# Kernel tuning notes

Hardware: AMD Instinct MI355X
Metric: run time of the kernel (lower is better)

The kernel has to match this reference:

```python
import jax, jax.numpy as jnp
import numpy as np

B, S, D = 1, 2048, 768
NH = 24; QNOPE = 32; QROPE = 16; QHD = QNOPE + QROPE; VHD = 32
QLR = 384; KVLR = 128
PK_HEADS = 4; KDIM = 128; NEXP = 16384; KNN = 8; EDIM = 768
ACT_HID = 24   # SwiGLU(dim=8): int(2*(4*8)/3)=21 -> rounded up to multiple_of=4 -> 24
SHARED_HID = 3072  # expert_dim * n_shared_experts = 768*4
EPS = 1e-5


def rms_norm(x, w):
    return x * jax.lax.rsqrt(jnp.mean(x * x, -1, keepdims=True) + EPS) * w


def swiglu(x, w1, w2, w3):
    return (jax.nn.silu(x @ w1.T) * (x @ w3.T)) @ w2.T


def rope(t, cos, sin):
    # t: (b, s, h, d); cos/sin: (s, d//2); rotate consecutive pairs (matches apply_rope)
    b, s, h, d = t.shape
    tr = t.reshape(b, s, h, d // 2, 2)
    r, i = tr[..., 0], tr[..., 1]
    c = cos[None, :, None, :]
    sn = sin[None, :, None, :]
    return jnp.stack([r * c - i * sn, r * sn + i * c], -1).reshape(b, s, h, d)


def setup_inputs() -> dict:
    key = jax.random.key(0)
    ks = jax.random.split(key, 20)
    rn = lambda k, shp, sc=0.02: jax.random.normal(k, shp, jnp.float32) * sc
    # RoPE tables: cos/sin of pos * inv_freq, dim = qk_rope_head_dim // 2 = 8
    inv = 1.0 / (10000.0 ** (jnp.arange(0, QROPE, 2, dtype=jnp.float32) / QROPE))
    f = jnp.arange(S, dtype=jnp.float32)[:, None] * inv[None, :]
    # causal additive mask (built here; spec fill 'zeros' is a placeholder)
    mask = jnp.where(jnp.tril(jnp.ones((S, S), bool)), 0.0, -1e9).astype(jnp.float32)[None, None]
    kb = float(1.0 / np.sqrt(KDIM))
    return {
        'x': rn(ks[0], (B, S, D), 1.0),
        'norm1_w': jnp.ones((D,), jnp.float32),
        'q_a_w': rn(ks[1], (QLR, D)),
        'q_a_ln_w': jnp.ones((QLR,), jnp.float32),
        'q_b_w': rn(ks[2], (NH * QHD, QLR)),
        'kv_a_w': rn(ks[3], (KVLR + QROPE, D)),
        'kv_a_ln_w': jnp.ones((KVLR,), jnp.float32),
        'kv_b_w': rn(ks[4], (NH * (QNOPE + VHD), KVLR)),
        'o_w': rn(ks[5], (D, NH * VHD)),
        'norm2_w': jnp.ones((D,), jnp.float32),
        'qp_w': rn(ks[6], (PK_HEADS * KDIM, D)),
        'qp_b': jnp.zeros((PK_HEADS * KDIM,), jnp.float32),
        'bn_g': jnp.ones((PK_HEADS * KDIM,), jnp.float32),
        'bn_b': jnp.zeros((PK_HEADS * KDIM,), jnp.float32),
        'keys': jax.random.uniform(ks[7], (PK_HEADS, NEXP, KDIM), jnp.float32, -kb, kb),
        'aw1': rn(ks[8], (ACT_HID, KNN), 0.1),
        'aw2': rn(ks[9], (KNN, ACT_HID), 0.1),
        'aw3': rn(ks[10], (ACT_HID, KNN), 0.1),
        'w_down': rn(ks[11], (NEXP, EDIM)),
        'w_up': rn(ks[12], (NEXP, EDIM)),
        'sw1': rn(ks[13], (SHARED_HID, D)),
        'sw2': rn(ks[14], (D, SHARED_HID)),
        'sw3': rn(ks[15], (SHARED_HID, D)),
        'mask': mask,
        'freqs_cos': jnp.cos(f),
        'freqs_sin': jnp.sin(f),
    }


def reference(x, norm1_w, q_a_w, q_a_ln_w, q_b_w, kv_a_w, kv_a_ln_w, kv_b_w, o_w,
              norm2_w, qp_w, qp_b, bn_g, bn_b, keys, aw1, aw2, aw3, w_down, w_up,
              sw1, sw2, sw3, mask, freqs_cos, freqs_sin):
    b, s, d = x.shape
    # ---- Attention (MLA-style, pre-norm) ----
    h_in = rms_norm(x, norm1_w)
    q = rms_norm(h_in @ q_a_w.T, q_a_ln_w) @ q_b_w.T
    q = q.reshape(b, s, NH, QHD).transpose(0, 2, 1, 3)            # (b, nh, s, 48)
    q_nope, q_pe = q[..., :QNOPE], q[..., QNOPE:]
    ckv = h_in @ kv_a_w.T                                         # (b, s, 144)
    compressed, k_pe = ckv[..., :KVLR], ckv[..., KVLR:]
    kv = (rms_norm(compressed, kv_a_ln_w) @ kv_b_w.T)
    kv = kv.reshape(b, s, NH, QNOPE + VHD).transpose(0, 2, 1, 3)  # (b, nh, s, 64)
    k_nope, v = kv[..., :QNOPE], kv[..., QNOPE:]
    q_pe = rope(q_pe.transpose(0, 2, 1, 3), freqs_cos, freqs_sin).transpose(0, 2, 1, 3)
    k_pe = rope(k_pe[:, :, None, :], freqs_cos, freqs_sin).transpose(0, 2, 1, 3)  # (b,1,s,16)
    q_states = jnp.concatenate([q_nope, q_pe], -1)                # (b, nh, s, 48)
    k_states = jnp.concatenate([k_nope, jnp.broadcast_to(k_pe, (b, NH, s, QROPE))], -1)
    att = jnp.einsum('bhqd,bhkd->bhqk', q_states, k_states) / np.sqrt(QHD).astype(np.float32) + mask
    probs = jax.nn.softmax(att, -1)
    ctx = jnp.einsum('bhqk,bhkd->bhqd', probs, v).transpose(0, 2, 1, 3).reshape(b, s, NH * VHD)
    h = x + ctx @ o_w.T
    # ---- ALL_MOE (product-key memory FFN) ----
    y = rms_norm(h, norm2_w)
    qflat = y.reshape(-1, d) @ qp_w.T + qp_b
    qflat = qflat / np.sqrt(1.0 + EPS).astype(np.float32) * bn_g + bn_b  # BatchNorm1d eval (mu=0, var=1)
    query = qflat.reshape(b * s, PK_HEADS, KDIM)
    sc = jnp.einsum('nhd,hkd->nhk', query, keys)                  # (b*s, heads, n_keys)
    top_s, top_i = jax.lax.top_k(sc, KNN)                         # (b*s, heads, knn)
    w = jax.nn.softmax(top_s, -1).reshape(b, s, PK_HEADS, KNN)
    idx = top_i.reshape(b, s, PK_HEADS, KNN)
    wd = w_down[idx]                                              # (b, s, heads, knn, D)
    wu = w_up[idx]
    z = jnp.einsum('btd,bthkd->bthk', y, wd)
    z = swiglu(z, aw1, aw2, aw3) * w
    moe = jnp.einsum('bthk,bthkd->btd', z, wu) + swiglu(y, sw1, sw2, sw3)
    return h + moe
```

## Files before the change

### kernel.cpp

```cpp
#include <hip/hip_runtime.h>
#include <hip/hip_bf16.h>
#include <hip/hip_fp16.h>

typedef __hip_bfloat16 bf16;

static constexpr int kS    = 2048;
static constexpr int kD    = 768;
static constexpr int kNH   = 24;
static constexpr int kQHD  = 48;
static constexpr int kVHD  = 32;
static constexpr int kQLR  = 384;
static constexpr int kKVLR = 128;
static constexpr int kPKH  = 4;
static constexpr int kNEXP = 16384;
static constexpr int kSH   = 3072;
static constexpr int kCH   = 768;
static constexpr float kEPS = 1e-5f;

__device__ __forceinline__ float b2f(bf16 v) { return __bfloat162float(v); }
__device__ __forceinline__ float silu_f(float x) { return x / (1.0f + expf(-x)); }

__device__ __forceinline__ float ldf(const void* p, size_t i, int m) {
  if (m == 0) return ((const float*)p)[i];
  if (m == 1) return b2f(((const bf16*)p)[i]);
  return __half2float(((const __half*)p)[i]);
}

__global__ void detect_kernel(const unsigned int* __restrict__ w, int* __restrict__ flag) {
  if (threadIdx.x == 0) {
    unsigned int v = w[0];
    flag[0] = (v == 0x3F800000u) ? 0 : ((v == 0x3C003C00u) ? 2 : 1);
  }
}

__global__ __launch_bounds__(256) void fill_kernel(float* __restrict__ out, float v, int n) {
  int i = blockIdx.x * 256 + threadIdx.x;
  if (i < n) out[i] = v;
}

__global__ __launch_bounds__(256) void rms_in_kernel(
    const void* __restrict__ in, const void* __restrict__ w,
    float* __restrict__ out, int cols, const int* __restrict__ dflag) {
  int m = dflag[0];
  int row = blockIdx.x;
  size_t base = (size_t)row * cols;
  __shared__ float red[256];
  float s = 0.f;
  for (int c = threadIdx.x; c < cols; c += 256) { float v = ldf(in, base + c, m); s += v * v; }
  red[threadIdx.x] = s; __syncthreads();
  for (int o = 128; o > 0; o >>= 1) {
    if (threadIdx.x < o) red[threadIdx.x] += red[threadIdx.x + o];
    __syncthreads();
  }
  float scale = rsqrtf(red[0] / cols + kEPS);
  for (int c = threadIdx.x; c < cols; c += 256)
    out[base + c] = ldf(in, base + c, m) * scale * ldf(w, c, m);
}

__global__ __launch_bounds__(256) void rms_f32_kernel(
    const float* __restrict__ in, int istride, const void* __restrict__ w,
    float* __restrict__ out, int cols, const int* __restrict__ dflag) {
  int m = dflag[0];
  int row = blockIdx.x;
  const float* r = in + (size_t)row * istride;
  __shared__ float red[256];
  float s = 0.f;
  for (int c = threadIdx.x; c < cols; c += 256) { float v = r[c]; s += v * v; }
  red[threadIdx.x] = s; __syncthreads();
  for (int o = 128; o > 0; o >>= 1) {
    if (threadIdx.x < o) red[threadIdx.x] += red[threadIdx.x + o];
    __syncthreads();
  }
  float scale = rsqrtf(red[0] / cols + kEPS);
  for (int c = threadIdx.x; c < cols; c += 256)
    out[(size_t)row * cols + c] = r[c] * scale * ldf(w, c, m);
}

template <bool ACC, int DT>
__device__ __forceinline__ void gemm_body(
    const float* __restrict__ A, int lda,
    const void* __restrict__ W, int ldw, int wrow0, int kofs,
    float* __restrict__ C, int ldc, int N, int K,
    float (*As)[68], float (*Ws)[68]) {
  int row0 = blockIdx.y * 64, col0 = blockIdx.x * 64;
  int tid = threadIdx.x;
  int tx = tid & 15, ty = tid >> 4;
  int am = tid >> 3, ak = (tid & 7) * 4;
  int hn = tid >> 2, hk = (tid & 3) * 8;

  float4 ra0, ra1, rw0, rw1;
  uint4 rh;

  auto fetch = [&](int k0) {
    ra0 = *(const float4*)(A + (size_t)(row0 + am) * lda + k0 + ak);
    ra1 = *(const float4*)(A + (size_t)(row0 + am + 32) * lda + k0 + ak);
    if constexpr (DT == 0) {
      const float* Wf = (const float*)W;
      int n0 = col0 + am, n1 = n0 + 32;
      float4 z = make_float4(0.f, 0.f, 0.f, 0.f);
      rw0 = (n0 < N) ? *(const float4*)(Wf + (size_t)(wrow0 + n0) * ldw + kofs + k0 + ak) : z;
      rw1 = (n1 < N) ? *(const float4*)(Wf + (size_t)(wrow0 + n1) * ldw + kofs + k0 + ak) : z;
    } else {
      int n = col0 + hn;
      if (n < N)
        rh = *(const uint4*)((const unsigned short*)W + (size_t)(wrow0 + n) * ldw + kofs + k0 + hk);
      else
        rh = make_uint4(0u, 0u, 0u, 0u);
    }
  };

  auto stage = [&]() {
    As[ak + 0][am] = ra0.x; As[ak + 1][am] = ra0.y;
    As[ak + 2][am] = ra0.z; As[ak + 3][am] = ra0.w;
    As[ak + 0][am + 32] = ra1.x; As[ak + 1][am + 32] = ra1.y;
    As[ak + 2][am + 32] = ra1.z; As[ak + 3][am + 32] = ra1.w;
    if constexpr (DT == 0) {
      Ws[ak + 0][am] = rw0.x; Ws[ak + 1][am] = rw0.y;
      Ws[ak + 2][am] = rw0.z; Ws[ak + 3][am] = rw0.w;
      Ws[ak + 0][am + 32] = rw1.x; Ws[ak + 1][am + 32] = rw1.y;
      Ws[ak + 2][am + 32] = rw1.z; Ws[ak + 3][am + 32] = rw1.w;
    } else if constexpr (DT == 1) {
      unsigned u[4] = {rh.x, rh.y, rh.z, rh.w};
#pragma unroll
      for (int i = 0; i < 4; i++) {
        Ws[hk + 2 * i][hn]     = __uint_as_float(u[i] << 16);
        Ws[hk + 2 * i + 1][hn] = __uint_as_float(u[i] & 0xFFFF0000u);
      }
    } else {
      unsigned u[4] = {rh.x, rh.y, rh.z, rh.w};
#pragma unroll
      for (int i = 0; i < 4; i++) {
        __half2 h2 = *(__half2*)&u[i];
        float2 f = __half22float2(h2);
        Ws[hk + 2 * i][hn]     = f.x;
        Ws[hk + 2 * i + 1][hn] = f.y;
      }
    }
  };

  float acc[4][4] = {};
  auto compute = [&]() {
#pragma unroll
    for (int kk = 0; kk < 32; kk++) {
      float4 a4 = *(const float4*)&As[kk][ty * 4];
      float4 b4 = *(const float4*)&Ws[kk][tx * 4];
      float a[4] = {a4.x, a4.y, a4.z, a4.w};
      float b[4] = {b4.x, b4.y, b4.z, b4.w};
#pragma unroll
      for (int i = 0; i < 4; i++)
#pragma unroll
        for (int j = 0; j < 4; j++) acc[i][j] += a[i] * b[j];
    }
  };

  fetch(0);
  stage();
  __syncthreads();
  for (int k0 = 32; k0 < K; k0 += 32) {
    fetch(k0);
    compute();
    __syncthreads();
    stage();
    __syncthreads();
  }
  compute();

#pragma unroll
  for (int i = 0; i < 4; i++)
#pragma unroll
    for (int j = 0; j < 4; j++) {
      int col = col0 + tx * 4 + j;
      if (col < N) {
        size_t idx = (size_t)(row0 + ty * 4 + i) * ldc + col;
        C[idx] = (ACC ? C[idx] : 0.f) + acc[i][j];
      }
    }
}

template <bool ACC>
__global__ __launch_bounds__(256) void gemm_kernel(
    const float* __restrict__ A, int lda,
    const void* __restrict__ W, int ldw, int wrow0, int kofs,
    float* __restrict__ C, int ldc,
    int M, int N, int K, const int* __restrict__ dflag) {
  __shared__ float As[32][68];
  __shared__ float Ws[32][68];
  int dm = dflag[0];
  if (dm == 1)      gemm_body<ACC, 1>(A, lda, W, ldw, wrow0, kofs, C, ldc, N, K, As, Ws);
  else if (dm == 0) gemm_body<ACC, 0>(A, lda, W, ldw, wrow0, kofs, C, ldc, N, K, As, Ws);
  else              gemm_body<ACC, 2>(A, lda, W, ldw, wrow0, kofs, C, ldc, N, K, As, Ws);
}

__global__ __launch_bounds__(192) void ropeq_kernel(
    float* __restrict__ q, const void* __restrict__ fc, const void* __restrict__ fs,
    const int* __restrict__ dflag) {
  int m = dflag[0];
  int s = blockIdx.x, t = threadIdx.x;
  int h = t >> 3, p = t & 7;
  float c = ldf(fc, s * 8 + p, m), sn = ldf(fs, s * 8 + p, m);
  size_t base = (size_t)s * (kNH * kQHD) + h * kQHD + 32 + 2 * p;
  float r = q[base], im = q[base + 1];
  q[base]     = r * c - im * sn;
  q[base + 1] = r * sn + im * c;
}

__global__ __launch_bounds__(256) void ropek_kernel(
    const float* __restrict__ ckv, const void* __restrict__ fc, const void* __restrict__ fs,
    float* __restrict__ kpe, const int* __restrict__ dflag) {
  int m = dflag[0];
  int i = blockIdx.x * 256 + threadIdx.x;
  if (i >= kS * 8) return;
  int s = i >> 3, p = i & 7;
  float c = ldf(fc, s * 8 + p, m), sn = ldf(fs, s * 8 + p, m);
  float r  = ckv[(size_t)s * 144 + 128 + 2 * p];
  float im = ckv[(size_t)s * 144 + 128 + 2 * p + 1];
  kpe[s * 16 + 2 * p]     = r * c - im * sn;
  kpe[s * 16 + 2 * p + 1] = r * sn + im * c;
}

__global__ __launch_bounds__(256) void attn_kernel(
    const float* __restrict__ q, const float* __restrict__ kv,
    const float* __restrict__ kpe, float* __restrict__ ctx) {
  constexpr int KT = 64;
  __shared__ float Ks[KT][52];
  __shared__ float Vs[KT][36];
  __shared__ float Pt[KT][33];
  __shared__ float Tm[8][32];
  __shared__ float Sm[8][32];
  __shared__ float Ms[32], Ls[32], Fs[32];
  int qt = blockIdx.x, h = blockIdx.y, t = threadIdx.x;
  int qi = t & 31, g = t >> 5;
  int qrow = qt * 32 + qi;

  float qreg[48];
  const float* qp = q + (size_t)qrow * (kNH * kQHD) + h * kQHD;
#pragma unroll
  for (int i = 0; i < 12; i++) {
    float4 v4 = *(const float4*)(qp + 4 * i);
    qreg[4 * i] = v4.x; qreg[4 * i + 1] = v4.y;
    qreg[4 * i + 2] = v4.z; qreg[4 * i + 3] = v4.w;
  }
  if (t < 32) { Ms[t] = -INFINITY; Ls[t] = 0.f; }
  float acc[4] = {0.f, 0.f, 0.f, 0.f};
  const float scale = 0.144337567297406f;
  int nt = (qt * 32 + 32 + KT - 1) / KT;

  int srow = t >> 2, spart = t & 3;
  for (int tile = 0; tile < nt; tile++) {
    int kbase = tile * KT;
    {
      const float* src = kv + (size_t)(kbase + srow) * (kNH * 64) + h * 64 + spart * 16;
      float4 a = ((const float4*)src)[0];
      float4 b = ((const float4*)src)[1];
      float4 c = ((const float4*)src)[2];
      float4 d = ((const float4*)src)[3];
      if (spart < 2) {
        float* dst = &Ks[srow][spart * 16];
        ((float4*)dst)[0] = a; ((float4*)dst)[1] = b;
        ((float4*)dst)[2] = c; ((float4*)dst)[3] = d;
      } else {
        float* dst = &Vs[srow][(spart - 2) * 16];
        ((float4*)dst)[0] = a; ((float4*)dst)[1] = b;
        ((float4*)dst)[2] = c; ((float4*)dst)[3] = d;
      }
      float4 pe = *(const float4*)(kpe + (size_t)(kbase + srow) * 16 + spart * 4);
      *(float4*)&Ks[srow][32 + spart * 4] = pe;
    }
    __syncthreads();

    float s[8]; float lmax = -INFINITY;
    int k0 = g * 8;
#pragma unroll
    for (int kk = 0; kk < 8; kk++) {
      float d = 0.f;
#pragma unroll
      for (int d4 = 0; d4 < 12; d4++) {
        float4 k4 = *(const float4*)&Ks[k0 + kk][4 * d4];
        d += k4.x * qreg[4 * d4];
        d += k4.y * qreg[4 * d4 + 1];
        d += k4.z * qreg[4 * d4 + 2];
        d += k4.w * qreg[4 * d4 + 3];
      }
      d *= scale;
      if (kbase + k0 + kk > qrow) d = -1e9f;
      s[kk] = d;
      lmax = fmaxf(lmax, d);
    }
    Tm[g][qi] = lmax;
    __syncthreads();

    if (t < 32) {
      float tm = Tm[0][t];
#pragma unroll
      for (int gg = 1; gg < 8; gg++) tm = fmaxf(tm, Tm[gg][t]);
      float mo = Ms[t];
      float mn = fmaxf(mo, tm);
      Fs[t] = expf(mo - mn);
      Ms[t] = mn;
    }
    __syncthreads();

    float mq = Ms[qi];
    float psum = 0.f;
#pragma unroll
    for (int kk = 0; kk < 8; kk++) {
      float e = expf(s[kk] - mq);
      Pt[k0 + kk][qi] = e;
      psum += e;
    }
    Sm[g][qi] = psum;
    __syncthreads();

    if (t < 32) {
      float ls = 0.f;
#pragma unroll
      for (int gg = 0; gg < 8; gg++) ls += Sm[gg][t];
      Ls[t] = Ls[t] * Fs[t] + ls;
    }

    float f = Fs[qi];
#pragma unroll
    for (int j = 0; j < 4; j++) acc[j] *= f;
    int vd0 = g * 4;
#pragma unroll 8
    for (int kk = 0; kk < KT; kk++) {
      float p = Pt[kk][qi];
      float4 v4 = *(const float4*)&Vs[kk][vd0];
      acc[0] += p * v4.x; acc[1] += p * v4.y;
      acc[2] += p * v4.z; acc[3] += p * v4.w;
    }
    __syncthreads();
  }
  float inv = 1.f / Ls[qi];
  float* op = ctx + (size_t)qrow * (kNH * kVHD) + h * kVHD + g * 4;
  op[0] = acc[0] * inv; op[1] = acc[1] * inv;
  op[2] = acc[2] * inv; op[3] = acc[3] * inv;
}

__global__ __launch_bounds__(256) void addx_kernel(
    const void* __restrict__ x, const float* __restrict__ o, float* __restrict__ h, int n,
    const int* __restrict__ dflag) {
  int m = dflag[0];
  int i = blockIdx.x * 256 + threadIdx.x;
  if (i < n) h[i] = ldf(x, i, m) + o[i];
}

__global__ __launch_bounds__(256) void bnq_kernel(
    const float* __restrict__ raw, const void* __restrict__ qp_b,
    const void* __restrict__ g, const void* __restrict__ b,
    float* __restrict__ out, int n, const int* __restrict__ dflag) {
  int m = dflag[0];
  int i = blockIdx.x * 256 + threadIdx.x;
  if (i >= n) return;
  int j = i & 511;
  const float invs = 0.9999950000374996f;
  out[i] = (raw[i] + ldf(qp_b, j, m)) * invs * ldf(g, j, m) + ldf(b, j, m);
}

__global__ __launch_bounds__(256) void convert_keys_kernel(
    const void* __restrict__ keys, float* __restrict__ kf, const int* __restrict__ dflag) {
  int m = dflag[0];
  size_t i = ((size_t)blockIdx.x * 256 + threadIdx.x) * 8;
  if (m == 0) {
    const float4* s = (const float4*)((const float*)keys + i);
    float4 a = s[0], b = s[1];
    *(float4*)(kf + i) = a;
    *(float4*)(kf + i + 4) = b;
  } else if (m == 1) {
    uint4 u = *(const uint4*)((const unsigned short*)keys + i);
    unsigned uu[4] = {u.x, u.y, u.z, u.w};
    float o[8];
#pragma unroll
    for (int j = 0; j < 4; j++) {
      o[2 * j]     = __uint_as_float(uu[j] << 16);
      o[2 * j + 1] = __uint_as_float(uu[j] & 0xFFFF0000u);
    }
    *(float4*)(kf + i)     = make_float4(o[0], o[1], o[2], o[3]);
    *(float4*)(kf + i + 4) = make_float4(o[4], o[5], o[6], o[7]);
  } else {
    uint4 u = *(const uint4*)((const unsigned short*)keys + i);
    unsigned uu[4] = {u.x, u.y, u.z, u.w};
    float o[8];
#pragma unroll
    for (int j = 0; j < 4; j++) {
      __half2 h2 = *(__half2*)&uu[j];
      float2 f = __half22float2(h2);
      o[2 * j] = f.x; o[2 * j + 1] = f.y;
    }
    *(float4*)(kf + i)     = make_float4(o[0], o[1], o[2], o[3]);
    *(float4*)(kf + i + 4) = make_float4(o[4], o[5], o[6], o[7]);
  }
}

__device__ __forceinline__ void pk_tail(
    float* tval, int* tidx, int w, int lane, int n, int h, int rblk,
    float* __restrict__ cv, int* __restrict__ ci,
    float (*ldsv)[64][9], int (*ldsi)[64][9]) {
#pragma unroll
  for (int k = 0; k < 8; k++) { ldsv[w][lane][k] = tval[k]; ldsi[w][lane][k] = tidx[k]; }
  __syncthreads();
  if (w == 0) {
#pragma unroll
    for (int ww = 1; ww < 4; ww++) {
#pragma unroll
      for (int k = 0; k < 8; k++) {
        float cs = ldsv[ww][lane][k]; int cidx = ldsi[ww][lane][k];
        if (cs > tval[7]) {
#pragma unroll
          for (int t = 0; t < 8; t++) {
            if (cs > tval[t]) {
              float tv = tval[t]; int ti = tidx[t];
              tval[t] = cs; tidx[t] = cidx;
              cs = tv; cidx = ti;
            }
          }
        }
      }
    }
    size_t base = ((size_t)(n * 4 + h) * 16 + rblk) * 8;
#pragma unroll
    for (int k = 0; k < 8; k++) { cv[base + k] = tval[k]; ci[base + k] = tidx[k]; }
  }
}

__global__ __launch_bounds__(256) void pk_score_f32_kernel(
    const float* __restrict__ query, const float* __restrict__ keysf,
    float* __restrict__ cv, int* __restrict__ ci) {
  __shared__ float ldsv[4][64][9];
  __shared__ int   ldsi[4][64][9];
  int b    = blockIdx.x;
  int w    = threadIdx.x >> 6, lane = threadIdx.x & 63;
  int rblk = b & 15;
  int h    = (b >> 4) & 3;
  int qb   = b >> 6;
  int n    = qb * 64 + lane;
  int r    = rblk * 4 + w;

  float qv[128];
  const float4* qp = (const float4*)(query + (size_t)n * 512 + h * 128);
#pragma unroll
  for (int i = 0; i < 32; i++) {
    float4 t = qp[i];
    qv[4 * i] = t.x; qv[4 * i + 1] = t.y; qv[4 * i + 2] = t.z; qv[4 * i + 3] = t.w;
  }

  float tval[8]; int tidx[8];
#pragma unroll
  for (int k = 0; k < 8; k++) { tval[k] = -INFINITY; tidx[k] = 0x7FFFFFFF; }

  const float4* hbase = (const float4*)(keysf + (size_t)h * kNEXP * 128);
  int e0 = r * 256;
  for (int e = 0; e < 256; e++) {
    int eu = __builtin_amdgcn_readfirstlane(e0 + e);
    const float4* row = hbase + (size_t)eu * 32;
    float acc = 0.f;
#pragma unroll
    for (int w4 = 0; w4 < 32; w4++) {
      float4 f4 = row[w4];
      acc += f4.x * qv[4 * w4];
      acc += f4.y * qv[4 * w4 + 1];
      acc += f4.z * qv[4 * w4 + 2];
      acc += f4.w * qv[4 * w4 + 3];
    }
    if (acc > tval[7]) {
      float cs = acc; int cidx = eu;
#pragma unroll
      for (int k = 0; k < 8; k++) {
        if (cs > tval[k]) {
          float tv = tval[k]; int ti = tidx[k];
          tval[k] = cs; tidx[k] = cidx;
          cs = tv; cidx = ti;
        }
      }
    }
  }
  pk_tail(tval, tidx, w, lane, n, h, rblk, cv, ci, ldsv, ldsi);
}

template<int M>
__device__ __forceinline__ void pk_score_body(
    const float* __restrict__ query, const void* __restrict__ keys,
    float* __restrict__ cv, int* __restrict__ ci,
    float (*ldsv)[64][9], int (*ldsi)[64][9]) {
  int b    = blockIdx.x;
  int w    = threadIdx.x >> 6, lane = threadIdx.x & 63;
  int rblk = b & 15;
  int h    = (b >> 4) & 3;
  int qb   = b >> 6;
  int n    = qb * 64 + lane;
  int r    = rblk * 4 + w;

  float qv[128];
  const float4* qp = (const float4*)(query + (size_t)n * 512 + h * 128);
#pragma unroll
  for (int i = 0; i < 32; i++) {
    float4 t = qp[i];
    qv[4 * i] = t.x; qv[4 * i + 1] = t.y; qv[4 * i + 2] = t.z; qv[4 * i + 3] = t.w;
  }

  float tval[8]; int tidx[8];
#pragma unroll
  for (int k = 0; k < 8; k++) { tval[k] = -INFINITY; tidx[k] = 0x7FFFFFFF; }

  int e0 = r * 256;
  for (int e = 0; e < 256; e++) {
    int eu = __builtin_amdgcn_readfirstlane(e0 + e);
    float acc = 0.f;
    if constexpr (M == 1) {
      const uint4* row = (const uint4*)((const unsigned*)keys + ((size_t)h * kNEXP + eu) * 64);
#pragma unroll
      for (int w4 = 0; w4 < 16; w4++) {
        uint4 u4 = row[w4];
        unsigned uu[4] = {u4.x, u4.y, u4.z, u4.w};
#pragma unroll
        for (int j = 0; j < 4; j++) {
          float flo = __uint_as_float(uu[j] << 16);
          float fhi = __uint_as_float(uu[j] & 0xFFFF0000u);
          acc += flo * qv[8 * w4 + 2 * j];
          acc += fhi * qv[8 * w4 + 2 * j + 1];
        }
      }
    } else if constexpr (M == 0) {
      const float4* row = (const float4*)((const float*)keys + ((size_t)h * kNEXP + eu) * 128);
#pragma unroll
      for (int w4 = 0; w4 < 32; w4++) {
        float4 f4 = row[w4];
        acc += f4.x * qv[4 * w4];
        acc += f4.y * qv[4 * w4 + 1];
        acc += f4.z * qv[4 * w4 + 2];
        acc += f4.w * qv[4 * w4 + 3];
      }
    } else {
      const uint4* row = (const uint4*)((const unsigned*)keys + ((size_t)h * kNEXP + eu) * 64);
#pragma unroll
      for (int w4 = 0; w4 < 16; w4++) {
        uint4 u4 = row[w4];
        unsigned uu[4] = {u4.x, u4.y, u4.z, u4.w};
#pragma unroll
        for (int j = 0; j < 4; j++) {
          float flo = __half2float(__ushort_as_half((unsigned short)(uu[j] & 0xFFFFu)));
          float fhi = __half2float(__ushort_as_half((unsigned short)(uu[j] >> 16)));
          acc += flo * qv[8 * w4 + 2 * j];
          acc += fhi * qv[8 * w4 + 2 * j + 1];
        }
      }
    }
    if (acc > tval[7]) {
      float cs = acc; int cidx = eu;
#pragma unroll
      for (int k = 0; k < 8; k++) {
        if (cs > tval[k]) {
          float tv = tval[k]; int ti = tidx[k];
          tval[k] = cs; tidx[k] = cidx;
          cs = tv; cidx = ti;
        }
      }
    }
  }
  pk_tail(tval, tidx, w, lane, n, h, rblk, cv, ci, ldsv, ldsi);
}

__global__ __launch_bounds__(256) void pk_score_kernel(
    const float* __restrict__ query, const void* __restrict__ keys,
    float* __restrict__ cv, int* __restrict__ ci, const int* __restrict__ dflag) {
  __shared__ float ldsv[4][64][9];
  __shared__ int   ldsi[4][64][9];
  int m = dflag[0];
  if (m == 1)      pk_score_body<1>(query, keys, cv, ci, ldsv, ldsi);
  else if (m == 0) pk_score_body<0>(query, keys, cv, ci, ldsv, ldsi);
  else             pk_score_body<2>(query, keys, cv, ci, ldsv, ldsi);
}

__global__ __launch_bounds__(256) void pk_merge_kernel(
    const float* __restrict__ cv, const int* __restrict__ ci,
    int* __restrict__ idx_out, float* __restrict__ w_out) {
  int gw   = blockIdx.x * 4 + (threadIdx.x >> 6);
  int lane = threadIdx.x & 63;
  size_t base = (size_t)gw * 128;
  float lv0 = cv[base + lane * 2],     lv1 = cv[base + lane * 2 + 1];
  int   li0 = ci[base + lane * 2],     li1 = ci[base + lane * 2 + 1];
  float wv[8]; int wi[8];
#pragma unroll
  for (int k = 0; k < 8; k++) {
    float bv = lv0; int bi = li0;
    if (lv1 > bv || (lv1 == bv && li1 < bi)) { bv = lv1; bi = li1; }
#pragma unroll
    for (int o = 32; o > 0; o >>= 1) {
      float ov = __shfl_xor(bv, o);
      int   oi = __shfl_xor(bi, o);
      if (ov > bv || (ov == bv && oi < bi)) { bv = ov; bi = oi; }
    }
    wv[k] = bv; wi[k] = bi;
    if (lv0 == bv && li0 == bi) lv0 = -INFINITY;
    if (lv1 == bv && li1 == bi) lv1 = -INFINITY;
  }
  if (lane == 0) {
    float mx = wv[0];
    float e[8]; float ss = 0.f;
#pragma unroll
    for (int k = 0; k < 8; k++) { e[k] = expf(wv[k] - mx); ss += e[k]; }
#pragma unroll
    for (int k = 0; k < 8; k++) {
      idx_out[(size_t)gw * 8 + k] = wi[k];
      w_out[(size_t)gw * 8 + k]   = e[k] / ss;
    }
  }
}

__global__ __launch_bounds__(64) void kz_kernel(
    const float* __restrict__ y, const int* __restrict__ idxb,
    const void* __restrict__ w_down, float* __restrict__ z, const int* __restrict__ dflag) {
  int m = dflag[0];
  int bid = blockIdx.x;
  int n = bid >> 5, e = bid & 31;
  int row = idxb[(size_t)n * 32 + e] & (kNEXP - 1);
  const float* yr = y + (size_t)n * kD;
  size_t wr = (size_t)row * kD;
  float acc = 0.f;
  for (int d = threadIdx.x; d < kD; d += 64) acc += yr[d] * ldf(w_down, wr + d, m);
  for (int o = 32; o > 0; o >>= 1) acc += __shfl_down(acc, o);
  if (threadIdx.x == 0) z[(size_t)n * 32 + e] = acc;
}

__global__ __launch_bounds__(256) void act_kernel(
    const float* __restrict__ z, const float* __restrict__ wsm,
    const void* __restrict__ aw1, const void* __restrict__ aw2, const void* __restrict__ aw3,
    float* __restrict__ z2, const int* __restrict__ dflag) {
  int m = dflag[0];
  int t = blockIdx.x * 256 + threadIdx.x;
  if (t >= kS * kPKH) return;
  const float* zp = z + (size_t)t * 8;
  float zz[8];
#pragma unroll
  for (int k = 0; k < 8; k++) zz[k] = zp[k];
  float u[24];
#pragma unroll
  for (int j = 0; j < 24; j++) {
    float a1 = 0.f, a3 = 0.f;
#pragma unroll
    for (int k = 0; k < 8; k++) {
      a1 += ldf(aw1, j * 8 + k, m) * zz[k];
      a3 += ldf(aw3, j * 8 + k, m) * zz[k];
    }
    u[j] = silu_f(a1) * a3;
  }
#pragma unroll
  for (int k = 0; k < 8; k++) {
    float o = 0.f;
#pragma unroll
    for (int j = 0; j < 24; j++) o += u[j] * ldf(aw2, k * 24 + j, m);
    z2[(size_t)t * 8 + k] = o * wsm[(size_t)t * 8 + k];
  }
}

__global__ __launch_bounds__(256) void moe_kernel(
    const float* __restrict__ z2, const int* __restrict__ idxb,
    const void* __restrict__ w_up, float* __restrict__ moe, const int* __restrict__ dflag) {
  int m = dflag[0];
  int n = blockIdx.x, tid = threadIdx.x;
  __shared__ float zs[32];
  __shared__ int   is[32];
  if (tid < 32) {
    zs[tid] = z2[(size_t)n * 32 + tid];
    is[tid] = idxb[(size_t)n * 32 + tid] & (kNEXP - 1);
  }
  __syncthreads();
  for (int d = tid; d < kD; d += 256) {
    float acc = 0.f;
#pragma unroll 8
    for (int e = 0; e < 32; e++) acc += zs[e] * ldf(w_up, (size_t)is[e] * kD + d, m);
    moe[(size_t)n * kD + d] = acc;
  }
}

__global__ __launch_bounds__(256) void silumul_kernel(
    float* __restrict__ g1, const float* __restrict__ g3, int n) {
  int i = blockIdx.x * 256 + threadIdx.x;
  if (i < n) g1[i] = silu_f(g1[i]) * g3[i];
}

__global__ __launch_bounds__(256) void combine_kernel(
    const float* __restrict__ h, const float* __restrict__ moe,
    float* __restrict__ out, int n) {
  int i = blockIdx.x * 256 + threadIdx.x;
  if (i < n) out[i] = h[i] + moe[i];
}

extern "C" void kernel_launch(void* const* d_in, const int* in_sizes, int n_in,
                              void* d_out, int out_size, void* d_ws, size_t ws_size,
                              hipStream_t stream) {
  float* out = (float*)d_out;
  dim3 b256(256);

  static const long long kExp[26] = {
    (long long)kS * kD, kD,
    (long long)kQLR * kD, kQLR,
    (long long)kNH * kQHD * kQLR,
    (long long)(kKVLR + 16) * kD, kKVLR,
    (long long)kNH * 64 * kKVLR,
    (long long)kD * kNH * kVHD, kD,
    (long long)kPKH * 128 * kD, kPKH * 128, kPKH * 128, kPKH * 128,
    (long long)kPKH * kNEXP * 128,
    24 * 8, 8 * 24, 24 * 8,
    (long long)kNEXP * kD, (long long)kNEXP * kD,
    (long long)kSH * kD, (long long)kD * kSH, (long long)kSH * kD,
    (long long)kS * kS, (long long)kS * 8, (long long)kS * 8,
  };
  int map[26];
  bool used[256] = {};
  bool ok = (n_in >= 26 && n_in <= 256);
  if (ok) {
    for (int j = 0; j < 26; j++) {
      int found = -1;
      for (int i = 0; i < n_in; i++)
        if (!used[i] && (long long)in_sizes[i] == kExp[j]) { found = i; break; }
      if (found < 0) { ok = false; break; }
      used[found] = true;
      map[j] = found;
    }
  }
  if (!ok) {
    fill_kernel<<<(out_size + 255) / 256, b256, 0, stream>>>(out, 100.0f, out_size);
    return;
  }

  const void* x        = d_in[map[0]];
  const void* norm1_w  = d_in[map[1]];
  const void* q_a_w    = d_in[map[2]];
  const void* q_a_ln_w = d_in[map[3]];
  const void* q_b_w    = d_in[map[4]];
  const void* kv_a_w   = d_in[map[5]];
  const void* kv_a_ln_w= d_in[map[6]];
  const void* kv_b_w   = d_in[map[7]];
  const void* o_w      = d_in[map[8]];
  const void* norm2_w  = d_in[map[9]];
  const void* qp_w     = d_in[map[10]];
  const void* qp_b     = d_in[map[11]];
  const void* bn_g     = d_in[map[12]];
  const void* bn_b     = d_in[map[13]];
  const void* keys     = d_in[map[14]];
  const void* aw1      = d_in[map[15]];
  const void* aw2      = d_in[map[16]];
  const void* aw3      = d_in[map[17]];
  const void* w_down   = d_in[map[18]];
  const void* w_up     = d_in[map[19]];
  const void* sw1      = d_in[map[20]];
  const void* sw2      = d_in[map[21]];
  const void* sw3      = d_in[map[22]];
  const void* fcos     = d_in[map[24]];
  const void* fsin     = d_in[map[25]];

  float* ws = (float*)d_ws;
  size_t off = 0;
  auto alloc = [&](size_t n) { float* p = ws + off; off += n; return p; };

  int*   dflag = (int*)alloc(16);
  float* slotA = alloc((size_t)kS * kD);
  float* slotB = alloc((size_t)kS * kQLR);
  float* slotC = alloc((size_t)kS * kNH * kQHD);
  float* ckv   = alloc((size_t)kS * 144);
  float* cn    = alloc((size_t)kS * kKVLR);
  float* kpe   = alloc((size_t)kS * 16);
  float* slotD = alloc((size_t)kS * kNH * 64);
  float* hbuf  = alloc((size_t)kS * kD);
  float* y     = alloc((size_t)kS * kD);
  size_t need_bytes = off * sizeof(float);
  if (ws_size < need_bytes) return;

  size_t nkeys = (size_t)kPKH * kNEXP * 128;
  float* keysf = ws + off;
  bool have_kf = (ws_size >= (off + nkeys) * sizeof(float));

  float* h_in  = slotA;
  float* qa    = slotB;
  float* qan   = hbuf;
  float* q     = slotC;
  float* kv    = slotD;
  float* ctx   = slotA;
  float* otmp  = slotC;
  float* qpraw = slotA;
  float* query = slotD + (size_t)kS * kD;
  int*   idxb  = (int*)slotB;
  float* wsm   = slotB + 65536;
  float* z     = slotB + 2 * 65536;
  float* z2    = slotB + 3 * 65536;
  float* moe   = slotD + (size_t)kS * kD;
  float* g1c   = slotC;
  float* g3c   = slotD;
  float* cand_v = slotA;
  int*   cand_i = (int*)slotC;

  detect_kernel<<<1, 64, 0, stream>>>((const unsigned int*)norm1_w, dflag);
  rms_in_kernel<<<kS, b256, 0, stream>>>(x, norm1_w, h_in, kD, dflag);
  gemm_kernel<false><<<dim3(6, 32), b256, 0, stream>>>(h_in, kD, q_a_w, kD, 0, 0, qa, kQLR, kS, kQLR, kD, dflag);
  rms_f32_kernel<<<kS, b256, 0, stream>>>(qa, kQLR, q_a_ln_w, qan, kQLR, dflag);
  gemm_kernel<false><<<dim3(18, 32), b256, 0, stream>>>(qan, kQLR, q_b_w, kQLR, 0, 0, q, kNH * kQHD, kS, kNH * kQHD, kQLR, dflag);
  gemm_kernel<false><<<dim3(3, 32), b256, 0, stream>>>(h_in, kD, kv_a_w, kD, 0, 0, ckv, 144, kS, 144, kD, dflag);
  rms_f32_kernel<<<kS, b256, 0, stream>>>(ckv, 144, kv_a_ln_w, cn, kKVLR, dflag);
  ropeq_kernel<<<kS, dim3(192), 0, stream>>>(q, fcos, fsin, dflag);
  ropek_kernel<<<(kS * 8 + 255) / 256, b256, 0, stream>>>(ckv, fcos, fsin, kpe, dflag);
  gemm_kernel<false><<<dim3(24, 32), b256, 0, stream>>>(cn, kKVLR, kv_b_w, kKVLR, 0, 0, kv, kNH * 64, kS, kNH * 64, kKVLR, dflag);
  if (have_kf)
    convert_keys_kernel<<<dim3((unsigned)(nkeys / 8 / 256)), b256, 0, stream>>>(keys, keysf, dflag);
  attn_kernel<<<dim3(kS / 32, kNH), b256, 0, stream>>>(q, kv, kpe, ctx);
  gemm_kernel<false><<<dim3(12, 32), b256, 0, stream>>>(ctx, kD, o_w, kD, 0, 0, otmp, kD, kS, kD, kD, dflag);
  addx_kernel<<<(kS * kD + 255) / 256, b256, 0, stream>>>(x, otmp, hbuf, kS * kD, dflag);
  rms_f32_kernel<<<kS, b256, 0, stream>>>(hbuf, kD, norm2_w, y, kD, dflag);
  gemm_kernel<false><<<dim3(8, 32), b256, 0, stream>>>(y, kD, qp_w, kD, 0, 0, qpraw, 512, kS, 512, kD, dflag);
  bnq_kernel<<<(kS * 512 + 255) / 256, b256, 0, stream>>>(qpraw, qp_b, bn_g, bn_b, query, kS * 512, dflag);
  if (have_kf)
    pk_score_f32_kernel<<<dim3(2048), b256, 0, stream>>>(query, keysf, cand_v, cand_i);
  else
    pk_score_kernel<<<dim3(2048), b256, 0, stream>>>(query, keys, cand_v, cand_i, dflag);
  pk_merge_kernel<<<dim3(2048), b256, 0, stream>>>(cand_v, cand_i, idxb, wsm);
  kz_kernel<<<kS * 32, dim3(64), 0, stream>>>(y, idxb, w_down, z, dflag);
  act_kernel<<<(kS * kPKH + 255) / 256, b256, 0, stream>>>(z, wsm, aw1, aw2, aw3, z2, dflag);
  moe_kernel<<<kS, b256, 0, stream>>>(z2, idxb, w_up, moe, dflag);
  for (int c = 0; c < kSH; c += kCH) {
    gemm_kernel<false><<<dim3(12, 32), b256, 0, stream>>>(y, kD, sw1, kD, c, 0, g1c, kCH, kS, kCH, kD, dflag);
    gemm_kernel<false><<<dim3(12, 32), b256, 0, stream>>>(y, kD, sw3, kD, c, 0, g3c, kCH, kS, kCH, kD, dflag);
    silumul_kernel<<<(kS * kCH + 255) / 256, b256, 0, stream>>>(g1c, g3c, kS * kCH);
    gemm_kernel<true><<<dim3(12, 32), b256, 0, stream>>>(g1c, kCH, sw2, kSH, 0, c, moe, kD, kS, kD, kCH, dflag);
  }
  combine_kernel<<<(kS * kD + 255) / 256, b256, 0, stream>>>(hbuf, moe, out, kS * kD);
}
```

Measured before the change: 3.204 ms.

## Add 64x128 register-prefetched GEMM and widen shared-expert chunks via keys workspace

Adds a new SIMT GEMM kernel with a 64x128 output tile, a 4x8 micro-tile per thread and register prefetch of the next K-slice while computing the current one. It is used for the q_b, kv_b and shared-expert gate/up projections. When the float keys workspace is available, the shared-expert intermediate chunk grows from 768 to 1536 columns by reusing that buffer as scratch, which halves the number of chunk iterations and kernel launches. The larger tile raises arithmetic intensity per shared-memory load but uses more registers and may lower occupancy. The kernel has no bounds checks, so it relies on dimensions dividing the tile evenly.

```diff
diff --git a/kernel.cpp b/kernel.cpp
--- a/kernel.cpp
+++ b/kernel.cpp
@@ -15,6 +15,7 @@
 static constexpr int kNEXP = 16384;
 static constexpr int kSH   = 3072;
 static constexpr int kCH   = 768;
+static constexpr int kCH2  = 1536;
 static constexpr float kEPS = 1e-5f;
 
 __device__ __forceinline__ float b2f(bf16 v) { return __bfloat162float(v); }
@@ -189,6 +190,131 @@
   if (dm == 1)      gemm_body<ACC, 1>(A, lda, W, ldw, wrow0, kofs, C, ldc, N, K, As, Ws);
   else if (dm == 0) gemm_body<ACC, 0>(A, lda, W, ldw, wrow0, kofs, C, ldc, N, K, As, Ws);
   else              gemm_body<ACC, 2>(A, lda, W, ldw, wrow0, kofs, C, ldc, N, K, As, Ws);
+}
+
+template <bool ACC, int DT>
+__device__ __forceinline__ void gemm3_body(
+    const float* __restrict__ A, int lda,
+    const void* __restrict__ W, int ldw, int wrow0, int kofs,
+    float* __restrict__ C, int ldc, int K,
+    float (*As)[68], float (*Ws)[132]) {
+  int row0 = blockIdx.y * 64, col0 = blockIdx.x * 128;
+  int tid = threadIdx.x;
+  int tx = tid & 15, ty = tid >> 4;
+  int ar = tid >> 2, ak = (tid & 3) * 8;
+  int wc = tid >> 1, wk = (tid & 1) * 16;
+
+  float4 ra0, ra1;
+  float4 rw0, rw1, rw2, rw3;
+  uint4 rh0, rh1;
+
+  auto fetch = [&](int k0) {
+    const float* ap = A + (size_t)(row0 + ar) * lda + k0 + ak;
+    ra0 = ((const float4*)ap)[0];
+    ra1 = ((const float4*)ap)[1];
+    if constexpr (DT == 0) {
+      const float* wp = (const float*)W + (size_t)(wrow0 + col0 + wc) * ldw + kofs + k0 + wk;
+      rw0 = ((const float4*)wp)[0]; rw1 = ((const float4*)wp)[1];
+      rw2 = ((const float4*)wp)[2]; rw3 = ((const float4*)wp)[3];
+    } else {
+      const unsigned short* wp =
+          (const unsigned short*)W + (size_t)(wrow0 + col0 + wc) * ldw + kofs + k0 + wk;
+      rh0 = ((const uint4*)wp)[0];
+      rh1 = ((const uint4*)wp)[1];
+    }
+  };
+
+  auto stage = [&]() {
+    As[ak + 0][ar] = ra0.x; As[ak + 1][ar] = ra0.y;
+    As[ak + 2][ar] = ra0.z; As[ak + 3][ar] = ra0.w;
+    As[ak + 4][ar] = ra1.x; As[ak + 5][ar] = ra1.y;
+    As[ak + 6][ar] = ra1.z; As[ak + 7][ar] = ra1.w;
+    if constexpr (DT == 0) {
+      Ws[wk +  0][wc] = rw0.x; Ws[wk +  1][wc] = rw0.y;
+      Ws[wk +  2][wc] = rw0.z; Ws[wk +  3][wc] = rw0.w;
+      Ws[wk +  4][wc] = rw1.x; Ws[wk +  5][wc] = rw1.y;
+      Ws[wk +  6][wc] = rw1.z; Ws[wk +  7][wc] = rw1.w;
+      Ws[wk +  8][wc] = rw2.x; Ws[wk +  9][wc] = rw2.y;
+      Ws[wk + 10][wc] = rw2.z; Ws[wk + 11][wc] = rw2.w;
+      Ws[wk + 12][wc] = rw3.x; Ws[wk + 13][wc] = rw3.y;
+      Ws[wk + 14][wc] = rw3.z; Ws[wk + 15][wc] = rw3.w;
+    } else if constexpr (DT == 1) {
+      unsigned u0[4] = {rh0.x, rh0.y, rh0.z, rh0.w};
+      unsigned u1[4] = {rh1.x, rh1.y, rh1.z, rh1.w};
+#pragma unroll
+      for (int i = 0; i < 4; i++) {
+        Ws[wk + 2 * i][wc]         = __uint_as_float(u0[i] << 16);
+        Ws[wk + 2 * i + 1][wc]     = __uint_as_float(u0[i] & 0xFFFF0000u);
+        Ws[wk + 8 + 2 * i][wc]     = __uint_as_float(u1[i] << 16);
+        Ws[wk + 8 + 2 * i + 1][wc] = __uint_as_float(u1[i] & 0xFFFF0000u);
+      }
+    } else {
+      unsigned u0[4] = {rh0.x, rh0.y, rh0.z, rh0.w};
+      unsigned u1[4] = {rh1.x, rh1.y, rh1.z, rh1.w};
+#pragma unroll
+      for (int i = 0; i < 4; i++) {
+        __half2 h0 = *(__half2*)&u0[i];
+        __half2 h1 = *(__half2*)&u1[i];
+        float2 f0 = __half22float2(h0);
+        float2 f1 = __half22float2(h1);
+        Ws[wk + 2 * i][wc]         = f0.x;
+        Ws[wk + 2 * i + 1][wc]     = f0.y;
+        Ws[wk + 8 + 2 * i][wc]     = f1.x;
+        Ws[wk + 8 + 2 * i + 1][wc] = f1.y;
+      }
+    }
+  };
+
+  float acc[4][8] = {};
+  auto compute = [&]() {
+#pragma unroll
+    for (int kk = 0; kk < 32; kk++) {
+      float4 a4 = *(const float4*)&As[kk][ty * 4];
+      float4 b0 = *(const float4*)&Ws[kk][tx * 8];
+      float4 b1 = *(const float4*)&Ws[kk][tx * 8 + 4];
+      float a[4] = {a4.x, a4.y, a4.z, a4.w};
+      float b[8] = {b0.x, b0.y, b0.z, b0.w, b1.x, b1.y, b1.z, b1.w};
+#pragma unroll
+      for (int i = 0; i < 4; i++)
+#pragma unroll
+        for (int j = 0; j < 8; j++) acc[i][j] += a[i] * b[j];
+    }
+  };
+
+  fetch(0);
+  stage();
+  __syncthreads();
+  for (int k0 = 32; k0 < K; k0 += 32) {
+    fetch(k0);
+    compute();
+    __syncthreads();
+    stage();
+    __syncthreads();
+  }
+  compute();
+
+#pragma unroll
+  for (int i = 0; i < 4; i++) {
+    size_t rbase = (size_t)(row0 + ty * 4 + i) * ldc + col0 + tx * 8;
+#pragma unroll
+    for (int j = 0; j < 8; j++) {
+      C[rbase + j] = (ACC ? C[rbase + j] : 0.f) + acc[i][j];
+    }
+  }
+}
+
+template <bool ACC>
+__global__ __launch_bounds__(256) void gemm3_kernel(
+    const float* __restrict__ A, int lda,
+    const void* __restrict__ W, int ldw, int wrow0, int kofs,
+    float* __restrict__ C, int ldc,
+    int K, const int* __restrict__ dflag) {
+  __shared__ float As[32][68];
+  __shared__ float Ws[32][132];
+  int dm = dflag[0];
+  if (dm == 1)      gemm3_body<ACC, 1>(A, lda, W, ldw, wrow0, kofs, C, ldc, K, As, Ws);
+  else if (dm == 0) gemm3_body<ACC, 0>(A, lda, W, ldw, wrow0, kofs, C, ldc, K, As, Ws);
+  else              gemm3_body<ACC, 2>(A, lda, W, ldw, wrow0, kofs, C, ldc, K, As, Ws);
 }
 
 __global__ __launch_bounds__(192) void ropeq_kernel(
@@ -785,8 +911,6 @@
   float* z     = slotB + 2 * 65536;
   float* z2    = slotB + 3 * 65536;
   float* moe   = slotD + (size_t)kS * kD;
-  float* g1c   = slotC;
-  float* g3c   = slotD;
   float* cand_v = slotA;
   int*   cand_i = (int*)slotC;
 
@@ -794,12 +918,12 @@
   rms_in_kernel<<<kS, b256, 0, stream>>>(x, norm1_w, h_in, kD, dflag);
   gemm_kernel<false><<<dim3(6, 32), b256, 0, stream>>>(h_in, kD, q_a_w, kD, 0, 0, qa, kQLR, kS, kQLR, kD, dflag);
   rms_f32_kernel<<<kS, b256, 0, stream>>>(qa, kQLR, q_a_ln_w, qan, kQLR, dflag);
-  gemm_kernel<false><<<dim3(18, 32), b256, 0, stream>>>(qan, kQLR, q_b_w, kQLR, 0, 0, q, kNH * kQHD, kS, kNH * kQHD, kQLR, dflag);
+  gemm3_kernel<false><<<dim3(9, 32), b256, 0, stream>>>(qan, kQLR, q_b_w, kQLR, 0, 0, q, kNH * kQHD, kQLR, dflag);
   gemm_kernel<false><<<dim3(3, 32), b256, 0, stream>>>(h_in, kD, kv_a_w, kD, 0, 0, ckv, 144, kS, 144, kD, dflag);
   rms_f32_kernel<<<kS, b256, 0, stream>>>(ckv, 144, kv_a_ln_w, cn, kKVLR, dflag);
   ropeq_kernel<<<kS, dim3(192), 0, stream>>>(q, fcos, fsin, dflag);
   ropek_kernel<<<(kS * 8 + 255) / 256, b256, 0, stream>>>(ckv, fcos, fsin, kpe, dflag);
-  gemm_kernel<false><<<dim3(24, 32), b256, 0, stream>>>(cn, kKVLR, kv_b_w, kKVLR, 0, 0, kv, kNH * 64, kS, kNH * 64, kKVLR, dflag);
+  gemm3_kernel<false><<<dim3(12, 32), b256, 0, stream>>>(cn, kKVLR, kv_b_w, kKVLR, 0, 0, kv, kNH * 64, kKVLR, dflag);
   if (have_kf)
     convert_keys_kernel<<<dim3((unsigned)(nkeys / 8 / 256)), b256, 0, stream>>>(keys, keysf, dflag);
   attn_kernel<<<dim3(kS / 32, kNH), b256, 0, stream>>>(q, kv, kpe, ctx);
@@ -816,11 +940,25 @@
   kz_kernel<<<kS * 32, dim3(64), 0, stream>>>(y, idxb, w_down, z, dflag);
   act_kernel<<<(kS * kPKH + 255) / 256, b256, 0, stream>>>(z, wsm, aw1, aw2, aw3, z2, dflag);
   moe_kernel<<<kS, b256, 0, stream>>>(z2, idxb, w_up, moe, dflag);
-  for (int c = 0; c < kSH; c += kCH) {
-    gemm_kernel<false><<<dim3(12, 32), b256, 0, stream>>>(y, kD, sw1, kD, c, 0, g1c, kCH, kS, kCH, kD, dflag);
-    gemm_kernel<false><<<dim3(12, 32), b256, 0, stream>>>(y, kD, sw3, kD, c, 0, g3c, kCH, kS, kCH, kD, dflag);
-    silumul_kernel<<<(kS * kCH + 255) / 256, b256, 0, stream>>>(g1c, g3c, kS * kCH);
-    gemm_kernel<true><<<dim3(12, 32), b256, 0, stream>>>(g1c, kCH, sw2, kSH, 0, c, moe, kD, kS, kD, kCH, dflag);
+
+  if (have_kf) {
+    float* g1c = keysf;
+    float* g3c = keysf + (size_t)kS * kCH2;
+    for (int c = 0; c < kSH; c += kCH2) {
+      gemm3_kernel<false><<<dim3(12, 32), b256, 0, stream>>>(y, kD, sw1, kD, c, 0, g1c, kCH2, kD, dflag);
+      gemm3_kernel<false><<<dim3(12, 32), b256, 0, stream>>>(y, kD, sw3, kD, c, 0, g3c, kCH2, kD, dflag);
+      silumul_kernel<<<(kS * kCH2 + 255) / 256, b256, 0, stream>>>(g1c, g3c, kS * kCH2);
+      gemm_kernel<true><<<dim3(12, 32), b256, 0, stream>>>(g1c, kCH2, sw2, kSH, 0, c, moe, kD, kS, kD, kCH2, dflag);
+    }
+  } else {
+    float* g1c = slotC;
+    float* g3c = slotD;
+    for (int c = 0; c < kSH; c += kCH) {
+      gemm_kernel<false><<<dim3(12, 32), b256, 0, stream>>>(y, kD, sw1, kD, c, 0, g1c, kCH, kS, kCH, kD, dflag);
+      gemm_kernel<false><<<dim3(12, 32), b256, 0, stream>>>(y, kD, sw3, kD, c, 0, g3c, kCH, kS, kCH, kD, dflag);
+      silumul_kernel<<<(kS * kCH + 255) / 256, b256, 0, stream>>>(g1c, g3c, kS * kCH);
+      gemm_kernel<true><<<dim3(12, 32), b256, 0, stream>>>(g1c, kCH, sw2, kSH, 0, c, moe, kD, kS, kD, kCH, dflag);
+    }
   }
   combine_kernel<<<(kS * kD + 255) / 256, b256, 0, stream>>>(hbuf, moe, out, kS * kD);
 }
```

Measured after the change: 2.892 ms. -9.7%, faster.
